# Kernel tuning notes

Measured on AMD Instinct MI355X. Metric: run time of the kernel, lower is better.

## Reference

```python
import jax, jax.numpy as jnp
import numpy as np

TOP_K = 8
ALPHA = 0.1
EPS = 1e-20


def setup_inputs() -> dict:
    key = jax.random.key(0)
    k1, k2 = jax.random.split(key)
    B, S, D, E = 4, 8192, 1024, 64
    hidden_states = jax.random.normal(k1, (B, S, D), dtype=jnp.float32)
    # kaiming_uniform_(a=sqrt(5)) on [E, D] -> bound = 1/sqrt(D)
    bound = 1.0 / np.sqrt(D)
    W = jax.random.uniform(k2, (E, D), dtype=jnp.float32, minval=-bound, maxval=bound)
    return {"hidden_states": hidden_states, "W": W}


def reference(hidden_states, W):
    B, S, D = hidden_states.shape
    E = W.shape[0]
    x = hidden_states.reshape(-1, D)                       # [T, D], T = B*S
    logits = jnp.einsum('td,ed->te', x, W)                 # [T, E]
    scores = jax.nn.softmax(logits, axis=-1)               # [T, E]
    top_k_weights, top_k_idx = jax.lax.top_k(scores, TOP_K)  # [T, K]
    # norm_topk_experts renormalization
    top_k_weights = top_k_weights / (top_k_weights.sum(axis=-1, keepdims=True) + EPS)
    # seq_aux loss: per-batch expert selection counts via scatter-add
    idx = top_k_idx.reshape(B, -1)                         # [B, S*K]
    ce = jnp.zeros((B, E), dtype=jnp.float32).at[jnp.arange(B)[:, None], idx].add(1.0)
    mean_scores = scores.reshape(B, S, E).mean(axis=1)     # [B, E]
    aux_loss = (ce * mean_scores).sum(axis=1).mean() * ALPHA
    return top_k_idx, top_k_weights, aux_loss
```

## Files before the change

### kernel.cpp

```cpp
#include <hip/hip_runtime.h>

#define TOKS   32768
#define NEXP   64
#define DDIM   1024
#define SEQ    8192
#define NBATCH 4
#define TPB    64
#define STR    68
#define CSTR   21

__global__ __launch_bounds__(256, 2) void moe_gate_main(
    const float* __restrict__ X, const float* __restrict__ W,
    float* __restrict__ out, float* __restrict__ gsum, float* __restrict__ gce,
    int* __restrict__ flag_cnt, int* __restrict__ flag_tok)
{
  __shared__ __align__(16) float xs[64 * STR];
  __shared__ __align__(16) float wsm[64 * STR];
  __shared__ float red[256];
  __shared__ float gmx[64];
  __shared__ float cval[64 * CSTR];
  __shared__ int   cidx[64 * CSTR];
  __shared__ int   hist[NEXP];

  const int tid = threadIdx.x;
  const int tok_base = blockIdx.x * TPB;
  const int bb = blockIdx.x >> 7;

  const int lc = tid & 15;
  const int lr = tid >> 4;
  const int l  = tid & 63;
  const int q  = tid >> 6;
  const int t0c = (l >> 3) * 8;
  const int e0c = (l & 7) * 8;
  const int dq = q * 16;

  float acc[8][8];
#pragma unroll
  for (int i = 0; i < 8; ++i)
#pragma unroll
    for (int j = 0; j < 8; ++j) acc[i][j] = 0.0f;

  float4 px[4], pw[4];
#pragma unroll
  for (int i = 0; i < 4; ++i) {
    px[i] = *(const float4*)(X + (size_t)(tok_base + 4 * lr + i) * DDIM + 4 * lc);
    pw[i] = *(const float4*)(W + (size_t)(4 * lr + i) * DDIM + 4 * lc);
  }

#pragma unroll 1
  for (int kt = 0; kt < DDIM / 64; ++kt) {
    __syncthreads();
#pragma unroll
    for (int j = 0; j < 4; ++j) {
      float4 vx = make_float4(((const float*)&px[0])[j], ((const float*)&px[1])[j],
                              ((const float*)&px[2])[j], ((const float*)&px[3])[j]);
      float4 vw = make_float4(((const float*)&pw[0])[j], ((const float*)&pw[1])[j],
                              ((const float*)&pw[2])[j], ((const float*)&pw[3])[j]);
      *(float4*)&xs[(4 * lc + j) * STR + 4 * lr] = vx;
      *(float4*)&wsm[(4 * lc + j) * STR + 4 * lr] = vw;
    }
    __syncthreads();
    if (kt + 1 < DDIM / 64) {
      const int dbase = (kt + 1) * 64;
#pragma unroll
      for (int i = 0; i < 4; ++i) {
        px[i] = *(const float4*)(X + (size_t)(tok_base + 4 * lr + i) * DDIM + dbase + 4 * lc);
        pw[i] = *(const float4*)(W + (size_t)(4 * lr + i) * DDIM + dbase + 4 * lc);
      }
    }
#pragma unroll
    for (int d = 0; d < 16; ++d) {
      const float* xr = &xs[(dq + d) * STR];
      const float* wr = &wsm[(dq + d) * STR];
      float xv[8], wv[8];
      *(float4*)&xv[0] = *(const float4*)(xr + t0c);
      *(float4*)&xv[4] = *(const float4*)(xr + t0c + 4);
      *(float4*)&wv[0] = *(const float4*)(wr + e0c);
      *(float4*)&wv[4] = *(const float4*)(wr + e0c + 4);
#pragma unroll
      for (int i = 0; i < 8; ++i)
#pragma unroll
        for (int j = 0; j < 8; ++j)
          acc[i][j] = fmaf(xv[i], wv[j], acc[i][j]);
    }
  }

  __syncthreads();
  if (q == 2) {
#pragma unroll
    for (int i = 0; i < 8; ++i) {
      *(float4*)&xs[(t0c + i) * STR + e0c]     = *(float4*)&acc[i][0];
      *(float4*)&xs[(t0c + i) * STR + e0c + 4] = *(float4*)&acc[i][4];
    }
  }
  if (q == 3) {
#pragma unroll
    for (int i = 0; i < 8; ++i) {
      *(float4*)&wsm[(t0c + i) * STR + e0c]     = *(float4*)&acc[i][0];
      *(float4*)&wsm[(t0c + i) * STR + e0c + 4] = *(float4*)&acc[i][4];
    }
  }
  __syncthreads();
  if (q == 0) {
#pragma unroll
    for (int i = 0; i < 8; ++i) {
      float4 a = *(const float4*)&xs[(t0c + i) * STR + e0c];
      float4 b = *(const float4*)&xs[(t0c + i) * STR + e0c + 4];
      acc[i][0] += a.x; acc[i][1] += a.y; acc[i][2] += a.z; acc[i][3] += a.w;
      acc[i][4] += b.x; acc[i][5] += b.y; acc[i][6] += b.z; acc[i][7] += b.w;
    }
  }
  if (q == 1) {
#pragma unroll
    for (int i = 0; i < 8; ++i) {
      float4 a = *(const float4*)&wsm[(t0c + i) * STR + e0c];
      float4 b = *(const float4*)&wsm[(t0c + i) * STR + e0c + 4];
      acc[i][0] += a.x; acc[i][1] += a.y; acc[i][2] += a.z; acc[i][3] += a.w;
      acc[i][4] += b.x; acc[i][5] += b.y; acc[i][6] += b.z; acc[i][7] += b.w;
    }
  }
  __syncthreads();
  if (q == 1) {
#pragma unroll
    for (int i = 0; i < 8; ++i) {
      *(float4*)&xs[(t0c + i) * STR + e0c]     = *(float4*)&acc[i][0];
      *(float4*)&xs[(t0c + i) * STR + e0c + 4] = *(float4*)&acc[i][4];
    }
  }
  __syncthreads();
  if (q == 0) {
#pragma unroll
    for (int i = 0; i < 8; ++i) {
      float4 a = *(const float4*)&xs[(t0c + i) * STR + e0c];
      float4 b = *(const float4*)&xs[(t0c + i) * STR + e0c + 4];
      acc[i][0] += a.x; acc[i][1] += a.y; acc[i][2] += a.z; acc[i][3] += a.w;
      acc[i][4] += b.x; acc[i][5] += b.y; acc[i][6] += b.z; acc[i][7] += b.w;
      *(float4*)&wsm[(t0c + i) * STR + e0c]     = *(float4*)&acc[i][0];
      *(float4*)&wsm[(t0c + i) * STR + e0c + 4] = *(float4*)&acc[i][4];
    }
    hist[l] = 0;
  }
  __syncthreads();

  float* logits  = wsm;
  float* scoresT = xs;
  const int t = l;

  float m = -__builtin_huge_valf();
#pragma unroll
  for (int e = 0; e < 16; ++e) m = fmaxf(m, logits[t * STR + q * 16 + e]);
  red[q * 64 + t] = m;
  __syncthreads();
  float gm = fmaxf(fmaxf(red[t], red[64 + t]), fmaxf(red[128 + t], red[192 + t]));
  if (q == 0) gmx[t] = gm;
  float z = 0.0f;
#pragma unroll
  for (int e = 0; e < 16; ++e) {
    float ev = expf(logits[t * STR + q * 16 + e] - gm);
    scoresT[(q * 16 + e) * STR + t] = ev;
    z += ev;
  }
  __syncthreads();
  red[q * 64 + t] = z;
  __syncthreads();
  float Z = red[t] + red[64 + t] + red[128 + t] + red[192 + t];
  float invZ = 1.0f / Z;
#pragma unroll
  for (int e = 0; e < 16; ++e) scoresT[(q * 16 + e) * STR + t] *= invZ;
  __syncthreads();

  {
    const int e = l, g = q;
    float s = 0.0f;
#pragma unroll
    for (int tt = 0; tt < 16; ++tt) s += scoresT[e * STR + g * 16 + tt];
    red[g * 64 + e] = s;
  }
  __syncthreads();
  if (tid < 64) {
    float tot = red[tid] + red[64 + tid] + red[128 + tid] + red[192 + tid];
    atomicAdd(&gsum[bb * 64 + tid], tot);
  }

  if (tid < 128) {
    const int h = tid >> 6;
    const int eb = h * 32;
#pragma unroll 1
    for (int k = 0; k < 9; ++k) {
      float mv = -1.0f; int mi = eb;
#pragma unroll 4
      for (int e = 0; e < 32; ++e) {
        float v = scoresT[(eb + e) * STR + t];
        if (v > mv) { mv = v; mi = eb + e; }
      }
      cval[t * CSTR + h * 9 + k] = mv;
      cidx[t * CSTR + h * 9 + k] = mi;
      scoresT[mi * STR + t] = -1.0f;
    }
  }
  __syncthreads();

  if (tid < 64) {
    float wv[9]; int wi[8];
#pragma unroll 1
    for (int k = 0; k < 9; ++k) {
      float mv = -1.0f; int mj = 0;
#pragma unroll 3
      for (int j = 0; j < 18; ++j) {
        float v = cval[t * CSTR + j];
        if (v > mv) { mv = v; mj = j; }
      }
      wv[k] = mv;
      if (k < 8) {
        wi[k] = cidx[t * CSTR + mj];
        atomicAdd(&hist[wi[k]], 1);
      }
      cval[t * CSTR + mj] = -1.0f;
    }
    bool flag = false;
#pragma unroll
    for (int k = 0; k < 8; ++k)
      if (wv[k + 1] >= wv[k] * (1.0f - 2.0e-5f)) flag = true;
    if (flag) {
      int p = atomicAdd(flag_cnt, 1);
      flag_tok[p] = tok_base + t;
    }
    double ed[8]; double den = 0.0;
#pragma unroll
    for (int k = 0; k < 8; ++k) {
      ed[k] = exp((double)logits[t * STR + wi[k]] - (double)gmx[t]);
      den += ed[k];
    }
    const size_t tg = (size_t)(tok_base + t);
    *(float4*)(out + tg * 8) =
        make_float4((float)wi[0], (float)wi[1], (float)wi[2], (float)wi[3]);
    *(float4*)(out + tg * 8 + 4) =
        make_float4((float)wi[4], (float)wi[5], (float)wi[6], (float)wi[7]);
    *(float4*)(out + (size_t)TOKS * 8 + tg * 8) =
        make_float4((float)(ed[0] / den), (float)(ed[1] / den),
                    (float)(ed[2] / den), (float)(ed[3] / den));
    *(float4*)(out + (size_t)TOKS * 8 + tg * 8 + 4) =
        make_float4((float)(ed[4] / den), (float)(ed[5] / den),
                    (float)(ed[6] / den), (float)(ed[7] / den));
  }
  __syncthreads();
  if (tid < 64) atomicAdd(&gce[bb * 64 + tid], (float)hist[tid]);
}

__global__ __launch_bounds__(256) void moe_refine(
    const float* __restrict__ X, const float* __restrict__ W,
    float* __restrict__ out, float* __restrict__ gce,
    const int* __restrict__ flag_cnt, const int* __restrict__ flag_tok)
{
  __shared__ __align__(16) float xrow[DDIM];
  __shared__ double part[4][NEXP];
  const int tid = threadIdx.x;
  const int n = *flag_cnt;
  const int e = tid & 63;
  const int c = tid >> 6;
#pragma unroll 1
  for (int it = blockIdx.x; it < n; it += 256) {
    const int tok = flag_tok[it];
    __syncthreads();
    *(float4*)&xrow[tid * 4] = *(const float4*)&X[(size_t)tok * DDIM + tid * 4];
    __syncthreads();
    const float* wr = W + (size_t)e * DDIM + c * 256;
    const float* xr = xrow + c * 256;
    double s0 = 0.0, s1 = 0.0, s2 = 0.0, s3 = 0.0;
#pragma unroll 4
    for (int j = 0; j < 256; j += 4) {
      s0 += (double)xr[j]     * (double)wr[j];
      s1 += (double)xr[j + 1] * (double)wr[j + 1];
      s2 += (double)xr[j + 2] * (double)wr[j + 2];
      s3 += (double)xr[j + 3] * (double)wr[j + 3];
    }
    part[c][e] = (s0 + s1) + (s2 + s3);
    __syncthreads();
    if (tid < 64) {
      double cur = (part[0][e] + part[1][e]) + (part[2][e] + part[3][e]);
      int wi[8]; double wl[8];
#pragma unroll 1
      for (int k = 0; k < 8; ++k) {
        double mv = cur; int mi = e;
#pragma unroll
        for (int off = 1; off < 64; off <<= 1) {
          double ov = __shfl_xor(mv, off);
          int    oi = __shfl_xor(mi, off);
          if (ov > mv || (ov == mv && oi < mi)) { mv = ov; mi = oi; }
        }
        wi[k] = mi; wl[k] = mv;
        if (e == mi) cur = -1.0e300;
      }
      if (e == 0) {
        int olde[8];
#pragma unroll
        for (int k = 0; k < 8; ++k) olde[k] = (int)out[(size_t)tok * 8 + k];
        double ex[8]; double den = 0.0;
#pragma unroll
        for (int k = 0; k < 8; ++k) { ex[k] = exp(wl[k] - wl[0]); den += ex[k]; }
#pragma unroll
        for (int k = 0; k < 8; ++k) {
          out[(size_t)tok * 8 + k] = (float)wi[k];
          out[(size_t)TOKS * 8 + (size_t)tok * 8 + k] = (float)(ex[k] / den);
        }
        const int bbb = tok >> 13;
#pragma unroll 1
        for (int k = 0; k < 8; ++k) {
          bool in_new = false, in_old = false;
          for (int j = 0; j < 8; ++j) {
            if (wi[j] == olde[k]) in_new = true;
            if (olde[j] == wi[k]) in_old = true;
          }
          if (!in_new) atomicAdd(&gce[bbb * 64 + olde[k]], -1.0f);
          if (!in_old) atomicAdd(&gce[bbb * 64 + wi[k]], 1.0f);
        }
      }
    }
  }
}

__global__ void moe_gate_aux(const float* __restrict__ gsum,
                             const float* __restrict__ gce,
                             float* __restrict__ out)
{
  __shared__ float r[256];
  const int tid = threadIdx.x;
  r[tid] = gce[tid] * gsum[tid];
  __syncthreads();
  for (int s = 128; s > 0; s >>= 1) {
    if (tid < s) r[tid] += r[tid + s];
    __syncthreads();
  }
  if (tid == 0)
    out[(size_t)TOKS * 16] = 0.1f * r[0] / ((float)SEQ * (float)NBATCH);
}

extern "C" void kernel_launch(void* const* d_in, const int* in_sizes, int n_in,
                              void* d_out, int out_size, void* d_ws, size_t ws_size,
                              hipStream_t stream)
{
  const float* X = (const float*)d_in[0];
  const float* W = (const float*)d_in[1];
  float* out  = (float*)d_out;
  float* gsum = (float*)d_ws;
  float* gce  = gsum + NBATCH * NEXP;
  int* flag_cnt = (int*)((char*)d_ws + 2048);
  int* flag_tok = (int*)((char*)d_ws + 2176);

  hipMemsetAsync(d_ws, 0, 2176, stream);
  moe_gate_main<<<TOKS / TPB, 256, 0, stream>>>(X, W, out, gsum, gce, flag_cnt, flag_tok);
  moe_refine<<<256, 256, 0, stream>>>(X, W, out, gce, flag_cnt, flag_tok);
  moe_gate_aux<<<1, 256, 0, stream>>>(gsum, gce, out);
}
```

Before: 242.4 us.

## Transpose W once and read it directly from global memory in gate GEMM

Adds a small pre-kernel that transposes W into a [D,E] workspace buffer. The main kernel then stages only X tiles in shared memory and reads each wavefront's 16-expert slice of W^T with wave-uniform addresses, which should turn into scalar or broadcast loads. Each thread now computes 16 logits for one token across the full K range, so the cross-wave split-K reduction through shared memory goes away. Occupancy is raised to 3 blocks per CU. The risks are an extra kernel launch and memset, and an inner loop bound by global or L2 reads of W instead of LDS reads.

```diff
diff --git a/kernel.cpp b/kernel.cpp
--- a/kernel.cpp
+++ b/kernel.cpp
@@ -9,13 +9,39 @@
 #define STR    68
 #define CSTR   21
 
-__global__ __launch_bounds__(256, 2) void moe_gate_main(
-    const float* __restrict__ X, const float* __restrict__ W,
+__global__ __launch_bounds__(256) void transpose_w(const float* __restrict__ W,
+                                                   float* __restrict__ WT)
+{
+  __shared__ __align__(16) float tile[64 * STR];
+  const int tid = threadIdx.x;
+  const int d0 = blockIdx.x * 64;
+  const int er = tid >> 2;
+#pragma unroll
+  for (int i = 0; i < 4; ++i) {
+    const int dq = (tid & 3) + 4 * i;
+    float4 v = *(const float4*)&W[(size_t)er * DDIM + d0 + dq * 4];
+    *(float4*)&tile[er * STR + dq * 4] = v;
+  }
+  __syncthreads();
+  const int dr = tid >> 2;
+#pragma unroll
+  for (int i = 0; i < 4; ++i) {
+    const int eq = (tid & 3) + 4 * i;
+    float4 v = make_float4(tile[(eq * 4 + 0) * STR + dr],
+                           tile[(eq * 4 + 1) * STR + dr],
+                           tile[(eq * 4 + 2) * STR + dr],
+                           tile[(eq * 4 + 3) * STR + dr]);
+    *(float4*)&WT[(size_t)(d0 + dr) * 64 + eq * 4] = v;
+  }
+}
+
+__global__ __launch_bounds__(256, 3) void moe_gate_main(
+    const float* __restrict__ X, const float* __restrict__ WT,
     float* __restrict__ out, float* __restrict__ gsum, float* __restrict__ gce,
     int* __restrict__ flag_cnt, int* __restrict__ flag_tok)
 {
   __shared__ __align__(16) float xs[64 * STR];
-  __shared__ __align__(16) float wsm[64 * STR];
+  __shared__ __align__(16) float lg[64 * STR];
   __shared__ float red[256];
   __shared__ float gmx[64];
   __shared__ float cval[64 * CSTR];
@@ -26,123 +52,59 @@
   const int tok_base = blockIdx.x * TPB;
   const int bb = blockIdx.x >> 7;
 
-  const int lc = tid & 15;
-  const int lr = tid >> 4;
-  const int l  = tid & 63;
-  const int q  = tid >> 6;
-  const int t0c = (l >> 3) * 8;
-  const int e0c = (l & 7) * 8;
-  const int dq = q * 16;
-
-  float acc[8][8];
-#pragma unroll
-  for (int i = 0; i < 8; ++i)
-#pragma unroll
-    for (int j = 0; j < 8; ++j) acc[i][j] = 0.0f;
-
-  float4 px[4], pw[4];
-#pragma unroll
-  for (int i = 0; i < 4; ++i) {
-    px[i] = *(const float4*)(X + (size_t)(tok_base + 4 * lr + i) * DDIM + 4 * lc);
-    pw[i] = *(const float4*)(W + (size_t)(4 * lr + i) * DDIM + 4 * lc);
-  }
-
-#pragma unroll 1
-  for (int kt = 0; kt < DDIM / 64; ++kt) {
-    __syncthreads();
-#pragma unroll
-    for (int j = 0; j < 4; ++j) {
-      float4 vx = make_float4(((const float*)&px[0])[j], ((const float*)&px[1])[j],
-                              ((const float*)&px[2])[j], ((const float*)&px[3])[j]);
-      float4 vw = make_float4(((const float*)&pw[0])[j], ((const float*)&pw[1])[j],
-                              ((const float*)&pw[2])[j], ((const float*)&pw[3])[j]);
-      *(float4*)&xs[(4 * lc + j) * STR + 4 * lr] = vx;
-      *(float4*)&wsm[(4 * lc + j) * STR + 4 * lr] = vw;
-    }
-    __syncthreads();
-    if (kt + 1 < DDIM / 64) {
+  const int l = tid & 63;
+  const int q = tid >> 6;
+  const int sr = tid >> 4;
+  const int sq = tid & 15;
+
+  const int ebase = __builtin_amdgcn_readfirstlane(q * 16);
+  const float* __restrict__ wt0 = WT + ebase;
+
+  float acc[16];
+#pragma unroll
+  for (int j = 0; j < 16; ++j) acc[j] = 0.0f;
+
+  float4 pf[4];
+#pragma unroll
+  for (int i = 0; i < 4; ++i)
+    pf[i] = *(const float4*)(X + (size_t)(tok_base + 16 * i + sr) * DDIM + sq * 4);
+
+#pragma unroll 1
+  for (int kt = 0; kt < 16; ++kt) {
+    __syncthreads();
+#pragma unroll
+    for (int i = 0; i < 4; ++i)
+      *(float4*)&xs[(16 * i + sr) * STR + sq * 4] = pf[i];
+    __syncthreads();
+    if (kt < 15) {
       const int dbase = (kt + 1) * 64;
 #pragma unroll
-      for (int i = 0; i < 4; ++i) {
-        px[i] = *(const float4*)(X + (size_t)(tok_base + 4 * lr + i) * DDIM + dbase + 4 * lc);
-        pw[i] = *(const float4*)(W + (size_t)(4 * lr + i) * DDIM + dbase + 4 * lc);
-      }
-    }
-#pragma unroll
-    for (int d = 0; d < 16; ++d) {
-      const float* xr = &xs[(dq + d) * STR];
-      const float* wr = &wsm[(dq + d) * STR];
-      float xv[8], wv[8];
-      *(float4*)&xv[0] = *(const float4*)(xr + t0c);
-      *(float4*)&xv[4] = *(const float4*)(xr + t0c + 4);
-      *(float4*)&wv[0] = *(const float4*)(wr + e0c);
-      *(float4*)&wv[4] = *(const float4*)(wr + e0c + 4);
-#pragma unroll
-      for (int i = 0; i < 8; ++i)
-#pragma unroll
-        for (int j = 0; j < 8; ++j)
-          acc[i][j] = fmaf(xv[i], wv[j], acc[i][j]);
-    }
-  }
-
-  __syncthreads();
-  if (q == 2) {
-#pragma unroll
-    for (int i = 0; i < 8; ++i) {
-      *(float4*)&xs[(t0c + i) * STR + e0c]     = *(float4*)&acc[i][0];
-      *(float4*)&xs[(t0c + i) * STR + e0c + 4] = *(float4*)&acc[i][4];
-    }
-  }
-  if (q == 3) {
-#pragma unroll
-    for (int i = 0; i < 8; ++i) {
-      *(float4*)&wsm[(t0c + i) * STR + e0c]     = *(float4*)&acc[i][0];
-      *(float4*)&wsm[(t0c + i) * STR + e0c + 4] = *(float4*)&acc[i][4];
-    }
-  }
-  __syncthreads();
-  if (q == 0) {
-#pragma unroll
-    for (int i = 0; i < 8; ++i) {
-      float4 a = *(const float4*)&xs[(t0c + i) * STR + e0c];
-      float4 b = *(const float4*)&xs[(t0c + i) * STR + e0c + 4];
-      acc[i][0] += a.x; acc[i][1] += a.y; acc[i][2] += a.z; acc[i][3] += a.w;
-      acc[i][4] += b.x; acc[i][5] += b.y; acc[i][6] += b.z; acc[i][7] += b.w;
-    }
-  }
-  if (q == 1) {
-#pragma unroll
-    for (int i = 0; i < 8; ++i) {
-      float4 a = *(const float4*)&wsm[(t0c + i) * STR + e0c];
-      float4 b = *(const float4*)&wsm[(t0c + i) * STR + e0c + 4];
-      acc[i][0] += a.x; acc[i][1] += a.y; acc[i][2] += a.z; acc[i][3] += a.w;
-      acc[i][4] += b.x; acc[i][5] += b.y; acc[i][6] += b.z; acc[i][7] += b.w;
-    }
-  }
-  __syncthreads();
-  if (q == 1) {
-#pragma unroll
-    for (int i = 0; i < 8; ++i) {
-      *(float4*)&xs[(t0c + i) * STR + e0c]     = *(float4*)&acc[i][0];
-      *(float4*)&xs[(t0c + i) * STR + e0c + 4] = *(float4*)&acc[i][4];
-    }
-  }
-  __syncthreads();
-  if (q == 0) {
-#pragma unroll
-    for (int i = 0; i < 8; ++i) {
-      float4 a = *(const float4*)&xs[(t0c + i) * STR + e0c];
-      float4 b = *(const float4*)&xs[(t0c + i) * STR + e0c + 4];
-      acc[i][0] += a.x; acc[i][1] += a.y; acc[i][2] += a.z; acc[i][3] += a.w;
-      acc[i][4] += b.x; acc[i][5] += b.y; acc[i][6] += b.z; acc[i][7] += b.w;
-      *(float4*)&wsm[(t0c + i) * STR + e0c]     = *(float4*)&acc[i][0];
-      *(float4*)&wsm[(t0c + i) * STR + e0c + 4] = *(float4*)&acc[i][4];
-    }
-    hist[l] = 0;
-  }
-  __syncthreads();
-
-  float* logits  = wsm;
+      for (int i = 0; i < 4; ++i)
+        pf[i] = *(const float4*)(X + (size_t)(tok_base + 16 * i + sr) * DDIM + dbase + sq * 4);
+    }
+    const float* __restrict__ wkt = wt0 + kt * 4096;
+#pragma unroll 2
+    for (int d4 = 0; d4 < 16; ++d4) {
+      float4 xq = *(const float4*)&xs[l * STR + d4 * 4];
+      const float* xf = (const float*)&xq;
+#pragma unroll
+      for (int dd = 0; dd < 4; ++dd) {
+        const float* __restrict__ wd = wkt + ((d4 * 4 + dd) << 6);
+        const float xv = xf[dd];
+#pragma unroll
+        for (int j = 0; j < 16; ++j)
+          acc[j] = fmaf(xv, wd[j], acc[j]);
+      }
+    }
+  }
+
+#pragma unroll
+  for (int j4 = 0; j4 < 4; ++j4)
+    *(float4*)&lg[l * STR + q * 16 + j4 * 4] = *(const float4*)&acc[j4 * 4];
+  if (tid < 64) hist[tid] = 0;
+  __syncthreads();
+
+  float* logits  = lg;
   float* scoresT = xs;
   const int t = l;
 
@@ -344,11 +306,14 @@
   float* out  = (float*)d_out;
   float* gsum = (float*)d_ws;
   float* gce  = gsum + NBATCH * NEXP;
-  int* flag_cnt = (int*)((char*)d_ws + 2048);
-  int* flag_tok = (int*)((char*)d_ws + 2176);
-
-  hipMemsetAsync(d_ws, 0, 2176, stream);
-  moe_gate_main<<<TOKS / TPB, 256, 0, stream>>>(X, W, out, gsum, gce, flag_cnt, flag_tok);
+  float* WT   = (float*)((char*)d_ws + 4096);
+  int* flag_cnt = (int*)((char*)d_ws + 4096 + 262144);
+  int* flag_tok = (int*)((char*)d_ws + 4096 + 262144 + 128);
+
+  hipMemsetAsync(d_ws, 0, 2048, stream);
+  hipMemsetAsync(flag_cnt, 0, 128, stream);
+  transpose_w<<<16, 256, 0, stream>>>(W, WT);
+  moe_gate_main<<<TOKS / TPB, 256, 0, stream>>>(X, WT, out, gsum, gce, flag_cnt, flag_tok);
   moe_refine<<<256, 256, 0, stream>>>(X, W, out, gce, flag_cnt, flag_tok);
   moe_gate_aux<<<1, 256, 0, stream>>>(gsum, gce, out);
 }
```

New measurement: 319.6 us. 31.9% more time.
